# Kernel tuning notes

Hardware: AMD Instinct MI355X
Metric: run time of the kernel (lower is better)

## Reference

```python
import jax, jax.numpy as jnp
import numpy as np

NUM_PARAMS = 3  # stand-in for crit._num_params


def unfold(x, k):
    # torch F.unfold(kernel=(k,k), padding=k//2, stride=1) -> (N, C*k*k, H*W)
    # channel-major, then kh, then kw (matches torch ordering)
    N, C, H, W = x.shape
    p = k // 2
    xp = jnp.pad(x, ((0, 0), (0, 0), (p, p), (p, p)))
    cols = [xp[:, :, i:i + H, j:j + W] for i in range(k) for j in range(k)]
    return jnp.stack(cols, axis=2).reshape(N, C * k * k, H * W)


def conv1x1(x, w, b):
    return jnp.einsum('nchw,oc->nohw', x, w) + b[None, :, None, None]


def mlp_1x1(x, wa, ba, wb, bb, wc, bc):
    x = jax.nn.leaky_relu(conv1x1(x, wa, ba), 0.2)
    x = jax.nn.leaky_relu(conv1x1(x, wb, bb), 0.2)
    return conv1x1(x, wc, bc)


def crit(y, p):
    # Stand-in 3-parameter per-channel Gaussian criterion (weight-logit, mu, log-sigma).
    N, _, H, W = p.shape
    C = y.shape[1]
    p = p.reshape(N, NUM_PARAMS, C, H, W)
    w, mu, log_s = p[:, 0], p[:, 1], p[:, 2]
    log_s = jnp.clip(log_s, -7.0, 7.0)
    nll = 0.5 * ((y - mu) * jnp.exp(-log_s)) ** 2 + log_s + 0.9189385 - jax.nn.log_sigmoid(w)
    return nll  # (N, C, H, W)


def masked_conv5(x, w, b):
    # MaskedConv2d type 'A': zero center and everything after it in raster order
    k = w.shape[-1]
    m = jnp.ones((k, k), w.dtype)
    m = m.at[k // 2, k // 2:].set(0.0)
    m = m.at[k // 2 + 1:, :].set(0.0)
    out = jax.lax.conv_general_dilated(x, w * m, (1, 1), [(k // 2, k // 2)] * 2,
                                       dimension_numbers=('NCHW', 'OIHW', 'NCHW'))
    return out + b[None, :, None, None]


def conv_ref(ref_unfold, w, H, W):
    # Conv2dUnfold.forward: masked weight applied as matmul on unfolded patches; no bias, fold(1,1)
    O, C, kH, kW = w.shape
    m = jnp.ones((kH, kW), w.dtype)
    m = m.at[kH // 2, kW // 2 + 1:].set(0.0)  # center kept here
    m = m.at[kH // 2 + 1:, :].set(0.0)
    wm = (w * m).reshape(O, -1)
    out = jnp.einsum('oc,nci->noi', wm, ref_unfold)
    return out.reshape(ref_unfold.shape[0], O, H, W)


def search_transfer(y_hat, y_prob, k=3):
    N, C, H, W = y_hat.shape
    HW = H * W
    m = jnp.ones((C, k, k), y_hat.dtype)  # causal patch mask (center zeroed)
    m = m.at[:, k // 2, k // 2:].set(0.0)
    m = m.at[:, k // 2 + 1:, :].set(0.0)
    mask_unfold = m.reshape(1, C * k * k, 1)
    u = unfold(y_hat, k) * mask_unfold
    u = u / jnp.maximum(jnp.linalg.norm(u, axis=1, keepdims=True), 1e-12)
    R = jnp.einsum('nci,ncj->nij', u, u)        # (N, HW, HW) patch self-correlation
    R = jnp.triu(R, k=1)                        # eval mode: strictly earlier positions only
    R_star = R.max(axis=1)                      # (N, HW)
    R_arg = jnp.argmax(R, axis=1)               # (N, HW)
    y_unf = unfold(y_hat, k)                    # (N, C*k*k, HW)
    ref_unfold = jnp.take_along_axis(y_unf, R_arg[:, None, :], axis=2)
    U_unf = jnp.take_along_axis(y_prob.reshape(N, 1, HW), R_arg[:, None, :], axis=2)
    S = R_star.reshape(N, 1, H, W)
    U = U_unf.reshape(N, 1, H, W)
    # eval-mode fixups for the first (causal-less) position
    S = S.at[:, :, 0, 0].set(1e-8)
    U = U.at[:, :, 0, 0].set(1e-8)
    ref_unfold = ref_unfold.at[:, :, 0].set(0.0)
    R_arg = R_arg.at[:, 0].set(-1)
    S = jnp.clip(S, 1e-8, 1.0)
    U = jnp.clip(U, 1e-8, 1.0)
    return S, U, ref_unfold, R_arg


def setup_inputs():
    key = jax.random.key(0)
    ks = jax.random.split(key, 32)

    def rn(i, shape, s=1.0):
        return jax.random.normal(ks[i], shape, jnp.float32) * s

    C, CH, NP_, CHN = 128, 128, NUM_PARAMS, 128
    N, H, W = 4, 64, 64
    return dict(
        y_quant=rn(0, (N, C, H, W)),
        z_feature=rn(1, (N, CH, H, W)),
        w_mask5=rn(2, (2 * C, C, 5, 5), 0.02), b_mask5=rn(3, (2 * C,), 0.02),
        w1a=rn(4, (CHN, 2 * C), 0.05), b1a=rn(5, (CHN,), 0.02),
        w1b=rn(6, (CHN, CHN), 0.05), b1b=rn(7, (CHN,), 0.02),
        w1c=rn(8, (NP_ * C, CHN), 0.05), b1c=rn(9, (NP_ * C,), 0.02),
        w_ref=rn(10, (2 * C, C, 3, 3), 0.02),
        w2a=rn(11, (CHN, 4 * C), 0.05), b2a=rn(12, (CHN,), 0.02),
        w2b=rn(13, (CHN, CHN), 0.05), b2b=rn(14, (CHN,), 0.02),
        w2c=rn(15, (NP_ * C, CHN), 0.05), b2c=rn(16, (NP_ * C,), 0.02),
        w3a=rn(17, (CHN, 4 * C + CH), 0.05), b3a=rn(18, (CHN,), 0.02),
        w3b=rn(19, (CHN, CHN), 0.05), b3b=rn(20, (CHN,), 0.02),
        w3c=rn(21, (NP_ * C, CHN), 0.05), b3c=rn(22, (NP_ * C,), 0.02),
    )


def reference(y_quant, z_feature, w_mask5, b_mask5,
              w1a, b1a, w1b, b1b, w1c, b1c, w_ref,
              w2a, b2a, w2b, b2b, w2c, b2c,
              w3a, b3a, w3b, b3b, w3c, b3c):
    N, C, H, W = y_quant.shape
    sg = jax.lax.stop_gradient
    local = masked_conv5(y_quant, w_mask5, b_mask5)
    para1_det = mlp_1x1(sg(local), w1a, b1a, w1b, b1b, w1c, b1c)
    y_prob1 = jnp.exp(-crit(y_quant, para1_det)).mean(axis=1, keepdims=True)
    S, U, ref_unfold, R_arg = search_transfer(sg(y_quant), sg(y_prob1))
    ref_feature = conv_ref(ref_unfold, w_ref, H, W)
    para1 = mlp_1x1(local, w1a, b1a, w1b, b1b, w1c, b1c)
    para2 = mlp_1x1(jnp.concatenate([local, ref_feature], 1), w2a, b2a, w2b, b2b, w2c, b2c)
    para2 = para2.reshape(N, NUM_PARAMS, C, H, W)
    para2 = para2.at[:, 0].add(jnp.log(S + 1e-8) + jnp.log(U + 1e-8))  # broadcast over C
    para2 = para2.reshape(N, NUM_PARAMS * C, H, W)
    para3 = mlp_1x1(jnp.concatenate([local, ref_feature, z_feature], 1), w3a, b3a, w3b, b3b, w3c, b3c)
    return para1, para2, para3, S, U, R_arg
```

## Files before the change

kernel.cpp:

```cpp
#include <hip/hip_runtime.h>
#include <cstdint>
#include <cstddef>

typedef unsigned short ushort_t;
typedef __attribute__((ext_vector_type(8))) short bf16x8;
typedef __attribute__((ext_vector_type(4))) float f32x4;

#if defined(__has_builtin)
#if __has_builtin(__builtin_amdgcn_global_load_lds)
#define HAVE_GLL 1
#endif
#endif

constexpr int NB = 4;
constexpr size_t OUT_P1 = 0;
constexpr size_t OUT_P2 = 6291456;
constexpr size_t OUT_P3 = 12582912;
constexpr size_t OUT_S  = 18874368;
constexpr size_t OUT_U  = 18890752;
constexpr size_t OUT_RA = 18907136;

constexpr size_t WS_SS    = 0;
constexpr size_t WS_RNORM = 16384;
constexpr size_t WS_YPROB = 32768;
// ... 51 lines not shown
static __device__ inline void gll16(const ushort_t* g, ushort_t* l) {
#ifdef HAVE_GLL
    __builtin_amdgcn_global_load_lds((const __attribute__((address_space(1))) void*)g,
                                     (__attribute__((address_space(3))) void*)l, 16, 0, 0);
#else
    uint4 v = *(const uint4*)g;
    *(uint4*)((char*)l + (threadIdx.x & 63) * 16) = v;
#endif
}

#define MFMA3(AH, AL, BH, BL, ACC) \
    ACC = __builtin_amdgcn_mfma_f32_16x16x32_bf16(AH, BH, ACC, 0, 0, 0); \
    ACC = __builtin_amdgcn_mfma_f32_16x16x32_bf16(AH, BL, ACC, 0, 0, 0); \
    ACC = __builtin_amdgcn_mfma_f32_16x16x32_bf16(AL, BH, ACC, 0, 0, 0);

__global__ __launch_bounds__(256) void repack_split(
    const float* __restrict__ w5, const float* __restrict__ wr,
    const float* __restrict__ w1a, const float* __restrict__ w1b, const float* __restrict__ w1c,
    const float* __restrict__ w2a, const float* __restrict__ w2b, const float* __restrict__ w2c,
    const float* __restrict__ w3a, const float* __restrict__ w3b, const float* __restrict__ w3c,
    ushort_t* __restrict__ WH, ushort_t* __restrict__ WL)
{
    int idx = blockIdx.x * 256 + threadIdx.x;
    if (idx >= 933888) return;
    float v; int i = idx;
    if (i < 393216) {
        int o = i / 1536, k = i % 1536; int tp = k >> 7, c = k & 127;
        int f = (int)((ENC5 >> (5 * tp)) & 31); int dh = (f & 3) - 2, dw = ((f >> 2) & 7) - 2;
        v = w5[((size_t)(o * 128 + c)) * 25 + (dh + 2) * 5 + (dw + 2)];
    } else if ((i -= 393216) < 163840) {
        int o = i / 640, k = i % 640; int tp = k >> 7, c = k & 127;
        int f = (int)((ENC3 >> (5 * tp)) & 31); int dh = (f & 3) - 2, dw = ((f >> 2) & 7) - 2;
        v = wr[((size_t)(o * 128 + c)) * 9 + (dh + 1) * 3 + (dw + 1)];
    }
    else if ((i -= 163840) < 32768) v = w1a[i];
    else if ((i -= 32768) < 16384) v = w1b[i];
    else if ((i -= 16384) < 49152) v = w1c[i];
    else if ((i -= 49152) < 32768) { int o = i >> 8, k = i & 255; v = w2a[o * 512 + k]; }
    else if ((i -= 32768) < 32768) { int o = i >> 8, k = i & 255; v = w2a[o * 512 + 256 + k]; }
    else if ((i -= 32768) < 16384) v = w2b[i];
    else if ((i -= 16384) < 49152) v = w2c[i];
    else if ((i -= 49152) < 49152) { int o = i / 384, k = i % 384; v = (k < 256) ? w3a[o * 640 + k] : w3a[o * 640 + 512 + (k - 256)]; }
    else if ((i -= 49152) < 32768) { int o = i >> 8, k = i & 255; v = w3a[o * 640 + 256 + k]; }
    else if ((i -= 32768) < 16384) v = w3b[i];
    else { i -= 16384; v = w3c[i]; }
    ushort_t h = f2bf_rne(v);
    WH[idx] = h;
    WL[idx] = f2bf_rne(v - bf2f(h));
}

__global__ __launch_bounds__(256) void padclear(float* __restrict__ dst)
{
    size_t i = (size_t)blockIdx.x * 256 + threadIdx.x;
    ((uint4*)dst)[i] = uint4{0u, 0u, 0u, 0u};
}

__global__ __launch_bounds__(256) void transsplit(const float* __restrict__ src,
    ushort_t* __restrict__ dh, ushort_t* __restrict__ dl, int pad)
{
    __shared__ float tile[128][17];
    int wc = blockIdx.x, h = blockIdx.y, n = blockIdx.z;
    int t = threadIdx.x;
    {
        int tw = t & 15, tc = t >> 4;
        #pragma unroll
        for (int r = 0; r < 8; ++r) {
            int c = tc * 8 + r;
            tile[c][tw] = src[((size_t)(n * 128 + c) << 12) + (h << 6) + wc * 16 + tw];
        }
    }
    __syncthreads();
    {
        int cc = t & 127, ww = t >> 7;
        #pragma unroll
        for (int r = 0; r < 8; ++r) {
            int w = ww * 8 + r;
            float v = tile[cc][w];
            size_t drow = pad ? ((size_t)n * 4624 + (size_t)(h + 1) * 68 + wc * 16 + w + 1)
                              : ((size_t)n * 4096 + (h << 6) + wc * 16 + w);
            ushort_t hh = f2bf_rne(v);
            dh[drow * 128 + cc] = hh;
            dl[drow * 128 + cc] = f2bf_rne(v - bf2f(hh));
        }
    }
}

__global__ __launch_bounds__(256) void sumsq_kernel(const float* __restrict__ y, float* __restrict__ ws)
{
    int idx = blockIdx.x * 256 + threadIdx.x;
    int n = idx >> 12, p = idx & 4095;
    const float* yp = y + (size_t)n * 128 * 4096 + p;
    float s = 0.f;
    for (int c = 0; c < 128; ++c) { float v = yp[(size_t)c * 4096]; s += v * v; }
    ws[WS_SS + idx] = s;
}

__global__ __launch_bounds__(256) void rnorm_kernel(float* __restrict__ ws)
{
    int idx = blockIdx.x * 256 + threadIdx.x;
    int n = idx >> 12, p = idx & 4095;
    int h = p >> 6, w = p & 63;
    const float* ss = ws + WS_SS + ((size_t)n << 12);
    float nsq = 0.f;
    if (h > 0 && w > 0)  nsq += ss[p - 65];
    if (h > 0)           nsq += ss[p - 64];
    if (h > 0 && w < 63) nsq += ss[p - 63];
    if (w > 0)           nsq += ss[p - 1];
    ws[WS_RNORM + idx] = 1.0f / fmaxf(sqrtf(nsq), 1e-12f);
}

__global__ __launch_bounds__(256) void vbuild_kernel(const ushort_t* __restrict__ ytpH,
                                                     const ushort_t* __restrict__ ytpL,
                                                     float* __restrict__ ws)
{
    size_t idx = (size_t)blockIdx.x * 256 + threadIdx.x;
    int k = (int)(idx & 511);
    int j = (int)((idx >> 12) & 4095);
    int kj = (int)((idx >> 9) & 7);
    (void)kj;
    j = (int)((idx >> 9) & 4095);
    int n = (int)(idx >> 21);
    int tp = k >> 7, c = k & 127;
    int h = j >> 6, w = j & 63;
    int dh, dw;
    if      (tp == 0) { dh = -1; dw = -1; }
    else if (tp == 1) { dh = -1; dw = 0;  }
    else if (tp == 2) { dh = -1; dw = 1;  }
    else              { dh = 0;  dw = -1; }
    size_t row = (size_t)n * 4624 + (size_t)(h + 1 + dh) * 68 + (w + 1 + dw);
    float v = (bf2f(ytpH[row * 128 + c]) + bf2f(ytpL[row * 128 + c]))
              * ws[WS_RNORM + ((size_t)n << 12) + j];
    ushort_t hi = f2bf_rne(v);
    ushort_t lo = f2bf_rne(v - bf2f(hi));
    ((ushort_t*)(ws + WS_VH))[idx] = hi;
    ((ushort_t*)(ws + WS_VL))[idx] = lo;
}

__global__ __launch_bounds__(256) void gram_mfma(const ushort_t* __restrict__ VH,
                                                 const ushort_t* __restrict__ VL,
                                                 float* __restrict__ pmax, int* __restrict__ parg)
{
    __shared__ __align__(16) ushort_t AsH[128 * 32];
    __shared__ __align__(16) ushort_t AsL[128 * 32];
    __shared__ __align__(16) ushort_t BsH[128 * 32];
// ... 92 lines not shown
        if (lane < 16) {
            sredv[wq_i * 128 + wq_j * 64 + ni * 16 + lane] = bv;
            sredi[wq_i * 128 + wq_j * 64 + ni * 16 + lane] = bi;
        }
    }
    __syncthreads();
    if (t < 128) {
        float v0 = sredv[t]; int i0 = sredi[t];
        float v1 = sredv[128 + t]; int i1 = sredi[128 + t];
        if (v1 > v0) { v0 = v1; i0 = i1; }
        pmax[(((size_t)n * 32 + ib) << 12) + jb * 128 + t] = v0;
        parg[(((size_t)n * 32 + ib) << 12) + jb * 128 + t] = i0;
    }
}

__global__ __launch_bounds__(128) void mfma_conv(
    const ushort_t* __restrict__ WH, const ushort_t* __restrict__ WL,
    const float* __restrict__ bias,
    const ushort_t* __restrict__ YH, const ushort_t* __restrict__ YL,
    uint64_t tapenc, int Ktot,
    ushort_t* __restrict__ outH, ushort_t* __restrict__ outL)
{
    __shared__ __align__(16) ushort_t AsH[64 * 32], AsL[64 * 32];
    __shared__ __align__(16) ushort_t BsH[128 * 32], BsL[128 * 32];
    int t = threadIdx.x, w = t >> 6, lane = t & 63;
    int p0 = blockIdx.x << 7, o0 = blockIdx.y << 6, n = blockIdx.z;
    int colq = lane >> 2, ks = lane & 3;
    int fr = lane & 15, kg = lane >> 4;
    int h0 = p0 >> 6;
    const ushort_t* yh = YH + (size_t)n * 4624 * 128;
    const ushort_t* yl = YL + (size_t)n * 4624 * 128;

    const ushort_t* aSrcH0 = WH + (size_t)(o0 + (2 * w + 0) * 16 + colq) * Ktot + ks * 8;
    const ushort_t* aSrcH1 = WH + (size_t)(o0 + (2 * w + 1) * 16 + colq) * Ktot + ks * 8;
    const ushort_t* aSrcL0 = WL + (size_t)(o0 + (2 * w + 0) * 16 + colq) * Ktot + ks * 8;
    const ushort_t* aSrcL1 = WL + (size_t)(o0 + (2 * w + 1) * 16 + colq) * Ktot + ks * 8;

    f32x4 acc[4][4];
    #pragma unroll
    for (int mi = 0; mi < 4; ++mi)
        #pragma unroll
        for (int ni = 0; ni < 4; ++ni) acc[mi][ni] = (f32x4){0.f, 0.f, 0.f, 0.f};

    for (int k0 = 0; k0 < Ktot; k0 += 32) {
        int tp = k0 >> 7, coff = (k0 & 127) + ks * 8;
        int f = (int)((tapenc >> (5 * tp)) & 31);
        int dh = (f & 3) - 2, dw = ((f >> 2) & 7) - 2;
        gll16(aSrcH0 + k0, &AsH[(2 * w + 0) * 512]);
        gll16(aSrcH1 + k0, &AsH[(2 * w + 1) * 512]);
        gll16(aSrcL0 + k0, &AsL[(2 * w + 0) * 512]);
        gll16(aSrcL1 + k0, &AsL[(2 * w + 1) * 512]);
        #pragma unroll
        for (int cb = 0; cb < 4; ++cb) {
            int c = w * 64 + cb * 16 + colq;
            int prow = (h0 + (c >> 6) + 1 + dh) * 68 + (c & 63) + 1 + dw;
            gll16(yh + (size_t)prow * 128 + coff, &BsH[(w * 4 + cb) * 512]);
            gll16(yl + (size_t)prow * 128 + coff, &BsL[(w * 4 + cb) * 512]);
        }
#ifdef HAVE_GLL
        asm volatile("s_waitcnt vmcnt(0)" ::: "memory");
#endif
        __syncthreads();
        bf16x8 ah[4], al[4], bh[4], bl[4];
        #pragma unroll
        for (int mi = 0; mi < 4; ++mi) {
            int col = mi * 16 + fr;
            ah[mi] = *(const bf16x8*)&AsH[col * 32 + kg * 8];
            al[mi] = *(const bf16x8*)&AsL[col * 32 + kg * 8];
        }
        #pragma unroll
// ... 18 lines not shown
        if (bias) bv = *(const f32x4*)&bias[og];
        #pragma unroll
        for (int ni = 0; ni < 4; ++ni) {
            int p = p0 + w * 64 + ni * 16 + fr;
            f32x4 v = acc[mi][ni] + bv;
            ushort_t h0s = f2bf_rne(v[0]), h1s = f2bf_rne(v[1]), h2s = f2bf_rne(v[2]), h3s = f2bf_rne(v[3]);
            size_t db = (((size_t)n << 12) + p) * 256 + og;
            *(uint2*)&outH[db] = make_uint2(h0s | ((uint32_t)h1s << 16), h2s | ((uint32_t)h3s << 16));
            ushort_t l0s = f2bf_rne(v[0] - bf2f(h0s)), l1s = f2bf_rne(v[1] - bf2f(h1s));
            ushort_t l2s = f2bf_rne(v[2] - bf2f(h2s)), l3s = f2bf_rne(v[3] - bf2f(h3s));
            *(uint2*)&outL[db] = make_uint2(l0s | ((uint32_t)l1s << 16), l2s | ((uint32_t)l3s << 16));
        }
    }
}

__global__ __launch_bounds__(128) void mfma_dense(
    const ushort_t* __restrict__ WH, const ushort_t* __restrict__ WL,
    const ushort_t* __restrict__ B0H, const ushort_t* __restrict__ B0L, int str0,
    int Ktot, float* __restrict__ outF)
{
    __shared__ __align__(16) ushort_t AsH[64 * 32], AsL[64 * 32];
    __shared__ __align__(16) ushort_t BsH[128 * 32], BsL[128 * 32];
    int t = threadIdx.x, w = t >> 6, lane = t & 63;
    int p0 = blockIdx.x << 7, o0 = blockIdx.y << 6, n = blockIdx.z;
    int colq = lane >> 2, ks = lane & 3;
    int fr = lane & 15, kg = lane >> 4;

    const ushort_t* aSrcH0 = WH + (size_t)(o0 + (2 * w + 0) * 16 + colq) * Ktot + ks * 8;
    const ushort_t* aSrcH1 = WH + (size_t)(o0 + (2 * w + 1) * 16 + colq) * Ktot + ks * 8;
    const ushort_t* aSrcL0 = WL + (size_t)(o0 + (2 * w + 0) * 16 + colq) * Ktot + ks * 8;
    const ushort_t* aSrcL1 = WL + (size_t)(o0 + (2 * w + 1) * 16 + colq) * Ktot + ks * 8;
    size_t brow[4];
    #pragma unroll
    for (int cb = 0; cb < 4; ++cb)
        brow[cb] = ((size_t)n << 12) + p0 + w * 64 + cb * 16 + colq;

    f32x4 acc[4][4];
    #pragma unroll
    for (int mi = 0; mi < 4; ++mi)
        #pragma unroll
        for (int ni = 0; ni < 4; ++ni) acc[mi][ni] = (f32x4){0.f, 0.f, 0.f, 0.f};

    for (int k0 = 0; k0 < Ktot; k0 += 32) {
        gll16(aSrcH0 + k0, &AsH[(2 * w + 0) * 512]);
        gll16(aSrcH1 + k0, &AsH[(2 * w + 1) * 512]);
        gll16(aSrcL0 + k0, &AsL[(2 * w + 0) * 512]);
        gll16(aSrcL1 + k0, &AsL[(2 * w + 1) * 512]);
        int kk = k0 + ks * 8;
        #pragma unroll
        for (int cb = 0; cb < 4; ++cb) {
            gll16(B0H + brow[cb] * str0 + kk, &BsH[(w * 4 + cb) * 512]);
            gll16(B0L + brow[cb] * str0 + kk, &BsL[(w * 4 + cb) * 512]);
        }
#ifdef HAVE_GLL
        asm volatile("s_waitcnt vmcnt(0)" ::: "memory");
#endif
        __syncthreads();
        bf16x8 ah[4], al[4], bh[4], bl[4];
        #pragma unroll
        for (int mi = 0; mi < 4; ++mi) {
            int col = mi * 16 + fr;
            ah[mi] = *(const bf16x8*)&AsH[col * 32 + kg * 8];
            al[mi] = *(const bf16x8*)&AsL[col * 32 + kg * 8];
        }
        #pragma unroll
        for (int ni = 0; ni < 4; ++ni) {
            int col = w * 64 + ni * 16 + fr;
// ... 21 lines not shown
}

struct MlpCfg {
    const ushort_t *waH, *waL; const float* ba; int Ka;
    const ushort_t *wbH, *wbL; const float* bb;
    const ushort_t *wcH, *wcL; const float* bc;
    const ushort_t *x0H, *x0L; int k0len, str0;
    const ushort_t *x1H, *x1L; int str1;
    const float* gatherP; int addLsu;
    float* outBase;
};

__global__ __launch_bounds__(256) void mlp_fused(MlpCfg c0, MlpCfg c1,
    const int* __restrict__ argi, const float* __restrict__ lsu)
{
    __shared__ __align__(16) ushort_t hbH[16384];
    __shared__ __align__(16) ushort_t hbL[16384];
    const MlpCfg c = blockIdx.y ? c1 : c0;
    int t = threadIdx.x, lane = t & 63, w = t >> 6;
    int fr = lane & 15, kg = lane >> 4;
    int p0 = blockIdx.x << 7, n = blockIdx.z;

    {
        int o_t = w >> 1, p_h = w & 1;
        f32x4 acc[4][4];
        #pragma unroll
        for (int mi = 0; mi < 4; ++mi)
            #pragma unroll
            for (int ni = 0; ni < 4; ++ni) acc[mi][ni] = (f32x4){0.f, 0.f, 0.f, 0.f};
        for (int k0 = 0; k0 < c.Ka; k0 += 32) {
            const ushort_t *xh, *xl; int kk, str;
            if (k0 < c.k0len) { xh = c.x0H; xl = c.x0L; kk = k0; str = c.str0; }
            else              { xh = c.x1H; xl = c.x1L; kk = k0 - c.k0len; str = c.str1; }
            kk += kg * 8;
            bf16x8 ah[4], al[4], bh[4], bl[4];
            #pragma unroll
            for (int ni = 0; ni < 4; ++ni) {
                size_t row = ((size_t)n << 12) + p0 + p_h * 64 + ni * 16 + fr;
                bh[ni] = *(const bf16x8*)&xh[row * str + kk];
                bl[ni] = *(const bf16x8*)&xl[row * str + kk];
            }
            #pragma unroll
            for (int mi = 0; mi < 4; ++mi) {
                size_t orow = (size_t)(o_t * 64 + mi * 16 + fr) * c.Ka + k0 + kg * 8;
                ah[mi] = *(const bf16x8*)&c.waH[orow];
                al[mi] = *(const bf16x8*)&c.waL[orow];
            }
            #pragma unroll
            for (int mi = 0; mi < 4; ++mi)
                #pragma unroll
                for (int ni = 0; ni < 4; ++ni) {
                    MFMA3(ah[mi], al[mi], bh[ni], bl[ni], acc[mi][ni]);
                }
        }
        #pragma unroll
        for (int mi = 0; mi < 4; ++mi) {
            int og = o_t * 64 + mi * 16 + kg * 4;
            f32x4 bv = *(const f32x4*)&c.ba[og];
            #pragma unroll
            for (int ni = 0; ni < 4; ++ni) {
                int p_loc = p_h * 64 + ni * 16 + fr;
                int p = p0 + p_loc;
                f32x4 v = acc[mi][ni] + bv;
                if (c.gatherP) {
                    int aj = argi[(n << 12) + p];
                    if (aj >= 0) v += *(const f32x4*)&c.gatherP[(((size_t)n << 12) + aj) * 128 + og];
                }
                #pragma unroll
                for (int r = 0; r < 4; ++r) v[r] = v[r] > 0.f ? v[r] : 0.2f * v[r];
                int osw = og ^ ((p_loc & 7) << 3);
                ushort_t h0s = f2bf_rne(v[0]), h1s = f2bf_rne(v[1]), h2s = f2bf_rne(v[2]), h3s = f2bf_rne(v[3]);
                *(uint2*)&hbH[p_loc * 128 + osw] = make_uint2(h0s | ((uint32_t)h1s << 16), h2s | ((uint32_t)h3s << 16));
                ushort_t l0s = f2bf_rne(v[0] - bf2f(h0s)), l1s = f2bf_rne(v[1] - bf2f(h1s));
                ushort_t l2s = f2bf_rne(v[2] - bf2f(h2s)), l3s = f2bf_rne(v[3] - bf2f(h3s));
                *(uint2*)&hbL[p_loc * 128 + osw] = make_uint2(l0s | ((uint32_t)l1s << 16), l2s | ((uint32_t)l3s << 16));
            }
        }
    }
    __syncthreads();
    {
        int o_t = w >> 1, p_h = w & 1;
        f32x4 acc[4][4];
        #pragma unroll
        for (int mi = 0; mi < 4; ++mi)
            #pragma unroll
            for (int ni = 0; ni < 4; ++ni) acc[mi][ni] = (f32x4){0.f, 0.f, 0.f, 0.f};
        for (int k0 = 0; k0 < 128; k0 += 32) {
            bf16x8 ah[4], al[4], bh[4], bl[4];
            #pragma unroll
            for (int ni = 0; ni < 4; ++ni) {
                int p_loc = p_h * 64 + ni * 16 + fr;
                int koff = (k0 + kg * 8) ^ ((p_loc & 7) << 3);
                bh[ni] = *(const bf16x8*)&hbH[p_loc * 128 + koff];
                bl[ni] = *(const bf16x8*)&hbL[p_loc * 128 + koff];
            }
            #pragma unroll
            for (int mi = 0; mi < 4; ++mi) {
                size_t orow = (size_t)(o_t * 64 + mi * 16 + fr) * 128 + k0 + kg * 8;
                ah[mi] = *(const bf16x8*)&c.wbH[orow];
                al[mi] = *(const bf16x8*)&c.wbL[orow];
            }
            #pragma unroll
            for (int mi = 0; mi < 4; ++mi)
                #pragma unroll
                for (int ni = 0; ni < 4; ++ni) {
                    MFMA3(ah[mi], al[mi], bh[ni], bl[ni], acc[mi][ni]);
                }
        }
        __syncthreads();
        #pragma unroll
        for (int mi = 0; mi < 4; ++mi) {
            int og = o_t * 64 + mi * 16 + kg * 4;
            f32x4 bv = *(const f32x4*)&c.bb[og];
            #pragma unroll
            for (int ni = 0; ni < 4; ++ni) {
                int p_loc = p_h * 64 + ni * 16 + fr;
                f32x4 v = acc[mi][ni] + bv;
                #pragma unroll
                for (int r = 0; r < 4; ++r) v[r] = v[r] > 0.f ? v[r] : 0.2f * v[r];
                int osw = og ^ ((p_loc & 7) << 3);
                ushort_t h0s = f2bf_rne(v[0]), h1s = f2bf_rne(v[1]), h2s = f2bf_rne(v[2]), h3s = f2bf_rne(v[3]);
                *(uint2*)&hbH[p_loc * 128 + osw] = make_uint2(h0s | ((uint32_t)h1s << 16), h2s | ((uint32_t)h3s << 16));
                ushort_t l0s = f2bf_rne(v[0] - bf2f(h0s)), l1s = f2bf_rne(v[1] - bf2f(h1s));
                ushort_t l2s = f2bf_rne(v[2] - bf2f(h2s)), l3s = f2bf_rne(v[3] - bf2f(h3s));
                *(uint2*)&hbL[p_loc * 128 + osw] = make_uint2(l0s | ((uint32_t)l1s << 16), l2s | ((uint32_t)l3s << 16));
            }
        }
    }
    __syncthreads();
    for (int it = 0; it < 3; ++it) {
        int u = w + 4 * it;
        int o_t = u >> 1, p_h = u & 1;
        f32x4 acc[4][4];
        #pragma unroll
        for (int mi = 0; mi < 4; ++mi)
            #pragma unroll
            for (int ni = 0; ni < 4; ++ni) acc[mi][ni] = (f32x4){0.f, 0.f, 0.f, 0.f};
        for (int k0 = 0; k0 < 128; k0 += 32) {
            bf16x8 ah[4], al[4], bh[4], bl[4];
            #pragma unroll
            for (int ni = 0; ni < 4; ++ni) {
                int p_loc = p_h * 64 + ni * 16 + fr;
                int koff = (k0 + kg * 8) ^ ((p_loc & 7) << 3);
                bh[ni] = *(const bf16x8*)&hbH[p_loc * 128 + koff];
                bl[ni] = *(const bf16x8*)&hbL[p_loc * 128 + koff];
            }
            #pragma unroll
            for (int mi = 0; mi < 4; ++mi) {
                size_t orow = (size_t)(o_t * 64 + mi * 16 + fr) * 128 + k0 + kg * 8;
                ah[mi] = *(const bf16x8*)&c.wcH[orow];
                al[mi] = *(const bf16x8*)&c.wcL[orow];
            }
            #pragma unroll
            for (int mi = 0; mi < 4; ++mi)
                #pragma unroll
                for (int ni = 0; ni < 4; ++ni) {
                    MFMA3(ah[mi], al[mi], bh[ni], bl[ni], acc[mi][ni]);
                }
        }
        #pragma unroll
        for (int mi = 0; mi < 4; ++mi) {
            int og = o_t * 64 + mi * 16 + kg * 4;
            f32x4 bv = *(const f32x4*)&c.bc[og];
            #pragma unroll
            for (int ni = 0; ni < 4; ++ni) {
                int p = p0 + p_h * 64 + ni * 16 + fr;
                f32x4 v = acc[mi][ni] + bv;
                if (c.addLsu && og < 128) {
                    float lv = lsu[(n << 12) + p];
                    v[0] += lv; v[1] += lv; v[2] += lv; v[3] += lv;
                }
                float* dst = c.outBase + (((size_t)(n * 384 + og)) << 12) + p;
                dst[0] = v[0]; dst[4096] = v[1]; dst[8192] = v[2]; dst[12288] = v[3];
            }
        }
    }
}

__global__ __launch_bounds__(256) void yprob_kernel(
    const float* __restrict__ out, const float* __restrict__ y, float* __restrict__ ws)
{
    int idx = blockIdx.x * 256 + threadIdx.x;
    int n = idx >> 12, p = idx & 4095;
    const float* pw = out + OUT_P1 + (size_t)n * 384 * 4096 + p;
    const float* pm = pw + (size_t)128 * 4096;
    const float* psv = pm + (size_t)128 * 4096;
    const float* yy = y + (size_t)n * 128 * 4096 + p;
    float accs = 0.f;
    for (int c = 0; c < 128; ++c) {
        float w  = pw[(size_t)c * 4096];
        float mu = pm[(size_t)c * 4096];
        float ls = psv[(size_t)c * 4096];
        ls = fminf(fmaxf(ls, -7.f), 7.f);
        float tt = (yy[(size_t)c * 4096] - mu) * expf(-ls);
        float lsig = (w >= 0.f) ? -log1pf(expf(-w)) : (w - log1pf(expf(w)));
        float nll = 0.5f * tt * tt + ls + 0.9189385f - lsig;
        accs += expf(-nll);
    }
    ws[WS_YPROB + idx] = accs * (1.0f / 128.0f);
}

__global__ __launch_bounds__(256) void finalize_kernel(float* __restrict__ ws, float* __restrict__ out)
{
    int idx = blockIdx.x * 256 + threadIdx.x;
    int n = idx >> 12, j = idx & 4095;
    float s, u; int a;
    if (j == 0) { s = 1e-8f; u = 1e-8f; a = -1; }
    else {
        float bv = -INFINITY; int bi = 0x7fffffff;
        const int* pai = (const int*)ws;
        int jbt = j >> 7;
        for (int ib = 0; ib <= jbt; ++ib) {
            float v = ws[WS_PMAX + (((size_t)n * 32 + ib) << 12) + j];
            int ii = pai[WS_PARG + (((size_t)n * 32 + ib) << 12) + j];
// ... 44 lines not shown
    const int* argi = (const int*)(ws) + WS_ARGI;

    ushort_t* wph = (ushort_t*)(ws + WS_WPK);
    ushort_t* wpl = wph + 933888;
    ushort_t* locH = (ushort_t*)(ws + WS_LOCH);
    ushort_t* locL = (ushort_t*)(ws + WS_LOCL);
    ushort_t* ftH  = (ushort_t*)(ws + WS_FTH);
    ushort_t* ftL  = (ushort_t*)(ws + WS_FTL);
    float* p2t = ws + WS_P2T;
    float* p3t = ws + WS_P3T;
    ushort_t* ztpH = (ushort_t*)(ws + WS_ZTPH);
    ushort_t* ztpL = (ushort_t*)(ws + WS_ZTPL);
    ushort_t* ytpH = (ushort_t*)(out + OS_YTPH);
    ushort_t* ytpL = (ushort_t*)(out + OS_YTPL);

    repack_split<<<3648, 256, 0, stream>>>(w5, wrf, w1a, w1b, w1c, w2a, w2b, w2c, w3a, w3b, w3c, wph, wpl);
    padclear<<<2312, 256, 0, stream>>>(out + OS_YTPH);
    transsplit<<<dim3(4, 64, NB), 256, 0, stream>>>(y, ytpH, ytpL, 1);
    transsplit<<<dim3(4, 64, NB), 256, 0, stream>>>(z, ztpH, ztpL, 0);
    sumsq_kernel<<<64, 256, 0, stream>>>(y, ws);
    rnorm_kernel<<<64, 256, 0, stream>>>(ws);
    vbuild_kernel<<<32768, 256, 0, stream>>>(ytpH, ytpL, ws);
    gram_mfma<<<dim3(528, NB), 256, 0, stream>>>((const ushort_t*)(ws + WS_VH), (const ushort_t*)(ws + WS_VL),
                                                 ws + WS_PMAX, (int*)(ws + WS_PARG));

    mfma_conv<<<dim3(32, 4, NB), 128, 0, stream>>>(wph + WP_W5, wpl + WP_W5, b5, ytpH, ytpL, ENC5, 1536, locH, locL);
    mfma_conv<<<dim3(32, 4, NB), 128, 0, stream>>>(wph + WP_WR, wpl + WP_WR, nullptr, ytpH, ytpL, ENC3, 640, ftH, ftL);
    mfma_dense<<<dim3(32, 2, NB), 128, 0, stream>>>(wph + WP_W2AR, wpl + WP_W2AR, ftH, ftL, 256, 256, p2t);
    mfma_dense<<<dim3(32, 2, NB), 128, 0, stream>>>(wph + WP_W3AR, wpl + WP_W3AR, ftH, ftL, 256, 256, p3t);

    MlpCfg m1;
    m1.waH = wph + WP_W1A; m1.waL = wpl + WP_W1A; m1.ba = b1a; m1.Ka = 256;
    m1.wbH = wph + WP_W1B; m1.wbL = wpl + WP_W1B; m1.bb = b1b;
    m1.wcH = wph + WP_W1C; m1.wcL = wpl + WP_W1C; m1.bc = b1c;
    m1.x0H = locH; m1.x0L = locL; m1.k0len = 256; m1.str0 = 256;
    m1.x1H = locH; m1.x1L = locL; m1.str1 = 256;
    m1.gatherP = nullptr; m1.addLsu = 0; m1.outBase = out + OUT_P1;
    mlp_fused<<<dim3(32, 1, NB), 256, 0, stream>>>(m1, m1, argi, ws + WS_LSU);

    yprob_kernel<<<64, 256, 0, stream>>>(out, y, ws);
    finalize_kernel<<<64, 256, 0, stream>>>(ws, out);

    MlpCfg m2;
    m2.waH = wph + WP_W2AL; m2.waL = wpl + WP_W2AL; m2.ba = b2a; m2.Ka = 256;
    m2.wbH = wph + WP_W2B; m2.wbL = wpl + WP_W2B; m2.bb = b2b;
    m2.wcH = wph + WP_W2C; m2.wcL = wpl + WP_W2C; m2.bc = b2c;
    m2.x0H = locH; m2.x0L = locL; m2.k0len = 256; m2.str0 = 256;
    m2.x1H = locH; m2.x1L = locL; m2.str1 = 256;
    m2.gatherP = p2t; m2.addLsu = 1; m2.outBase = out + OUT_P2;
    MlpCfg m3;
    m3.waH = wph + WP_W3ALZ; m3.waL = wpl + WP_W3ALZ; m3.ba = b3a; m3.Ka = 384;
    m3.wbH = wph + WP_W3B; m3.wbL = wpl + WP_W3B; m3.bb = b3b;
    m3.wcH = wph + WP_W3C; m3.wcL = wpl + WP_W3C; m3.bc = b3c;
    m3.x0H = locH; m3.x0L = locL; m3.k0len = 256; m3.str0 = 256;
    m3.x1H = ztpH; m3.x1L = ztpL; m3.str1 = 128;
    m3.gatherP = p3t; m3.addLsu = 0; m3.outBase = out + OUT_P3;
    mlp_fused<<<dim3(32, 2, NB), 256, 0, stream>>>(m2, m3, argi, ws + WS_LSU);

    (void)in_sizes; (void)n_in; (void)out_size; (void)ws_size;
}
```

Before: 623.4 us.

## Merge prep and conv launches, widen reductions, halve MLP tile for more blocks

Fuses the weight repack, pad clearing and both transposes into one prep kernel, clearing only the border rows of a now 2-wide padded y buffer. Merges the two conv GEMMs and the two dense GEMMs into single launches. Splits the sumsq and yprob channel reductions across four thread groups with a shared-memory reduction and a grid four times larger. Halves the MLP pixel tile to double the grid and cut LDS use. The goal is fewer launches and better GPU occupancy on these small kernels, at the cost of extra index logic and per-block weight reloads in the MLP.

Result: faster. 517.8 us (-16.9%).

```diff
diff --git a/kernel.cpp b/kernel.cpp
--- a/kernel.cpp
+++ b/kernel.cpp
@@ -89,53 +89,65 @@
     ACC = __builtin_amdgcn_mfma_f32_16x16x32_bf16(AH, BL, ACC, 0, 0, 0); \
     ACC = __builtin_amdgcn_mfma_f32_16x16x32_bf16(AL, BH, ACC, 0, 0, 0);
 
-__global__ __launch_bounds__(256) void repack_split(
+__global__ __launch_bounds__(256) void prep_fused(
     const float* __restrict__ w5, const float* __restrict__ wr,
     const float* __restrict__ w1a, const float* __restrict__ w1b, const float* __restrict__ w1c,
     const float* __restrict__ w2a, const float* __restrict__ w2b, const float* __restrict__ w2c,
     const float* __restrict__ w3a, const float* __restrict__ w3b, const float* __restrict__ w3c,
-    ushort_t* __restrict__ WH, ushort_t* __restrict__ WL)
-{
-    int idx = blockIdx.x * 256 + threadIdx.x;
-    if (idx >= 933888) return;
-    float v; int i = idx;
-    if (i < 393216) {
-        int o = i / 1536, k = i % 1536; int tp = k >> 7, c = k & 127;
-        int f = (int)((ENC5 >> (5 * tp)) & 31); int dh = (f & 3) - 2, dw = ((f >> 2) & 7) - 2;
-        v = w5[((size_t)(o * 128 + c)) * 25 + (dh + 2) * 5 + (dw + 2)];
-    } else if ((i -= 393216) < 163840) {
-        int o = i / 640, k = i % 640; int tp = k >> 7, c = k & 127;
-        int f = (int)((ENC3 >> (5 * tp)) & 31); int dh = (f & 3) - 2, dw = ((f >> 2) & 7) - 2;
-        v = wr[((size_t)(o * 128 + c)) * 9 + (dh + 1) * 3 + (dw + 1)];
-    }
-    else if ((i -= 163840) < 32768) v = w1a[i];
-    else if ((i -= 32768) < 16384) v = w1b[i];
-    else if ((i -= 16384) < 49152) v = w1c[i];
-    else if ((i -= 49152) < 32768) { int o = i >> 8, k = i & 255; v = w2a[o * 512 + k]; }
-    else if ((i -= 32768) < 32768) { int o = i >> 8, k = i & 255; v = w2a[o * 512 + 256 + k]; }
-    else if ((i -= 32768) < 16384) v = w2b[i];
-    else if ((i -= 16384) < 49152) v = w2c[i];
-    else if ((i -= 49152) < 49152) { int o = i / 384, k = i % 384; v = (k < 256) ? w3a[o * 640 + k] : w3a[o * 640 + 512 + (k - 256)]; }
-    else if ((i -= 49152) < 32768) { int o = i >> 8, k = i & 255; v = w3a[o * 640 + 256 + k]; }
-    else if ((i -= 32768) < 16384) v = w3b[i];
-    else { i -= 16384; v = w3c[i]; }
-    ushort_t h = f2bf_rne(v);
-    WH[idx] = h;
-    WL[idx] = f2bf_rne(v - bf2f(h));
-}
-
-__global__ __launch_bounds__(256) void padclear(float* __restrict__ dst)
-{
-    size_t i = (size_t)blockIdx.x * 256 + threadIdx.x;
-    ((uint4*)dst)[i] = uint4{0u, 0u, 0u, 0u};
-}
-
-__global__ __launch_bounds__(256) void transsplit(const float* __restrict__ src,
-    ushort_t* __restrict__ dh, ushort_t* __restrict__ dl, int pad)
+    const float* __restrict__ y, const float* __restrict__ z,
+    ushort_t* __restrict__ WH, ushort_t* __restrict__ WL,
+    ushort_t* __restrict__ ytpH, ushort_t* __restrict__ ytpL,
+    ushort_t* __restrict__ ztpH, ushort_t* __restrict__ ztpL)
 {
     __shared__ float tile[128][17];
-    int wc = blockIdx.x, h = blockIdx.y, n = blockIdx.z;
-    int t = threadIdx.x;
+    int b = blockIdx.x, t = threadIdx.x;
+    if (b < 3648) {
+        int idx = b * 256 + t;
+        if (idx >= 933888) return;
+        float v; int i = idx;
+        if (i < 393216) {
+            int o = i / 1536, k = i % 1536; int tp = k >> 7, c = k & 127;
+            int f = (int)((ENC5 >> (5 * tp)) & 31); int dh = (f & 3) - 2, dw = ((f >> 2) & 7) - 2;
+            v = w5[((size_t)(o * 128 + c)) * 25 + (dh + 2) * 5 + (dw + 2)];
+        } else if ((i -= 393216) < 163840) {
+            int o = i / 640, k = i % 640; int tp = k >> 7, c = k & 127;
+            int f = (int)((ENC3 >> (5 * tp)) & 31); int dh = (f & 3) - 2, dw = ((f >> 2) & 7) - 2;
+            v = wr[((size_t)(o * 128 + c)) * 9 + (dh + 1) * 3 + (dw + 1)];
+        }
+        else if ((i -= 163840) < 32768) v = w1a[i];
+        else if ((i -= 32768) < 16384) v = w1b[i];
+        else if ((i -= 16384) < 49152) v = w1c[i];
+        else if ((i -= 49152) < 32768) { int o = i >> 8, k = i & 255; v = w2a[o * 512 + k]; }
+        else if ((i -= 32768) < 32768) { int o = i >> 8, k = i & 255; v = w2a[o * 512 + 256 + k]; }
+        else if ((i -= 32768) < 16384) v = w2b[i];
+        else if ((i -= 16384) < 49152) v = w2c[i];
+        else if ((i -= 49152) < 49152) { int o = i / 384, k = i % 384; v = (k < 256) ? w3a[o * 640 + k] : w3a[o * 640 + 512 + (k - 256)]; }
+        else if ((i -= 49152) < 32768) { int o = i >> 8, k = i & 255; v = w3a[o * 640 + 256 + k]; }
+        else if ((i -= 32768) < 16384) v = w3b[i];
+        else { i -= 16384; v = w3c[i]; }
+        ushort_t h = f2bf_rne(v);
+        WH[idx] = h;
+        WL[idx] = f2bf_rne(v - bf2f(h));
+        return;
+    }
+    if (b < 3912) {
+        int slot = (b - 3648) * 8 + (t >> 5);
+        int n = slot / 528, rp = slot % 528;
+        int r, wcol;
+        if (rp < 272) { int x = rp / 68; r = x + ((x >> 1) << 6); wcol = rp % 68; }
+        else { int q = rp - 272; r = 2 + (q >> 2); int x = q & 3; wcol = x + ((x >> 1) << 6); }
+        size_t row = (size_t)n * 4624 + (size_t)r * 68 + wcol;
+        int lane = t & 31;
+        ushort_t* dst = ((lane >> 4) ? ytpL : ytpH) + row * 128;
+        ((uint4*)dst)[lane & 15] = uint4{0u, 0u, 0u, 0u};
+        return;
+    }
+    int b2, pad;
+    const float* src;
+    ushort_t *dh_, *dl_;
+    if (b < 4936) { b2 = b - 3912; pad = 1; src = y; dh_ = ytpH; dl_ = ytpL; }
+    else          { b2 = b - 4936; pad = 0; src = z; dh_ = ztpH; dl_ = ztpL; }
+    int wc = b2 & 3, h = (b2 >> 2) & 63, n = b2 >> 8;
     {
         int tw = t & 15, tc = t >> 4;
         #pragma unroll
@@ -151,23 +163,30 @@
         for (int r = 0; r < 8; ++r) {
             int w = ww * 8 + r;
             float v = tile[cc][w];
-            size_t drow = pad ? ((size_t)n * 4624 + (size_t)(h + 1) * 68 + wc * 16 + w + 1)
+            size_t drow = pad ? ((size_t)n * 4624 + (size_t)(h + 2) * 68 + wc * 16 + w + 2)
                               : ((size_t)n * 4096 + (h << 6) + wc * 16 + w);
             ushort_t hh = f2bf_rne(v);
-            dh[drow * 128 + cc] = hh;
-            dl[drow * 128 + cc] = f2bf_rne(v - bf2f(hh));
+            dh_[drow * 128 + cc] = hh;
+            dl_[drow * 128 + cc] = f2bf_rne(v - bf2f(hh));
         }
     }
 }
 
 __global__ __launch_bounds__(256) void sumsq_kernel(const float* __restrict__ y, float* __restrict__ ws)
 {
-    int idx = blockIdx.x * 256 + threadIdx.x;
-    int n = idx >> 12, p = idx & 4095;
-    const float* yp = y + (size_t)n * 128 * 4096 + p;
+    __shared__ float red[4][64];
+    int n = blockIdx.y, t = threadIdx.x;
+    int pl = t & 63, cg = t >> 6;
+    int p = (blockIdx.x << 6) + pl;
+    const float* yp = y + ((size_t)(n * 128 + cg * 32) << 12) + p;
     float s = 0.f;
-    for (int c = 0; c < 128; ++c) { float v = yp[(size_t)c * 4096]; s += v * v; }
-    ws[WS_SS + idx] = s;
+    #pragma unroll 8
+    for (int c = 0; c < 32; ++c) { float v = yp[(size_t)c << 12]; s = fmaf(v, v, s); }
+    red[cg][pl] = s;
+    __syncthreads();
+    if (t < 64)
+        ws[WS_SS + ((size_t)n << 12) + (blockIdx.x << 6) + t] =
+            red[0][t] + red[1][t] + red[2][t] + red[3][t];
 }
 
 __global__ __launch_bounds__(256) void rnorm_kernel(float* __restrict__ ws)
@@ -190,10 +209,7 @@
 {
     size_t idx = (size_t)blockIdx.x * 256 + threadIdx.x;
     int k = (int)(idx & 511);
-    int j = (int)((idx >> 12) & 4095);
-    int kj = (int)((idx >> 9) & 7);
-    (void)kj;
-    j = (int)((idx >> 9) & 4095);
+    int j = (int)((idx >> 9) & 4095);
     int n = (int)(idx >> 21);
     int tp = k >> 7, c = k & 127;
     int h = j >> 6, w = j & 63;
@@ -202,7 +218,7 @@
     else if (tp == 1) { dh = -1; dw = 0;  }
     else if (tp == 2) { dh = -1; dw = 1;  }
     else              { dh = 0;  dw = -1; }
-    size_t row = (size_t)n * 4624 + (size_t)(h + 1 + dh) * 68 + (w + 1 + dw);
+    size_t row = (size_t)n * 4624 + (size_t)(h + 2 + dh) * 68 + (w + 2 + dw);
     float v = (bf2f(ytpH[row * 128 + c]) + bf2f(ytpL[row * 128 + c]))
               * ws[WS_RNORM + ((size_t)n << 12) + j];
     ushort_t hi = f2bf_rne(v);
@@ -325,17 +341,28 @@
     }
 }
 
-__global__ __launch_bounds__(128) void mfma_conv(
-    const ushort_t* __restrict__ WH, const ushort_t* __restrict__ WL,
-    const float* __restrict__ bias,
+__global__ __launch_bounds__(128) void conv_merged(
+    const ushort_t* __restrict__ W5H, const ushort_t* __restrict__ W5L, const float* __restrict__ b5,
+    const ushort_t* __restrict__ WrH, const ushort_t* __restrict__ WrL,
     const ushort_t* __restrict__ YH, const ushort_t* __restrict__ YL,
-    uint64_t tapenc, int Ktot,
-    ushort_t* __restrict__ outH, ushort_t* __restrict__ outL)
+    ushort_t* __restrict__ locH, ushort_t* __restrict__ locL,
+    ushort_t* __restrict__ ftH, ushort_t* __restrict__ ftL)
 {
     __shared__ __align__(16) ushort_t AsH[64 * 32], AsL[64 * 32];
     __shared__ __align__(16) ushort_t BsH[128 * 32], BsL[128 * 32];
+    int by = blockIdx.y;
+    bool is5 = by < 4;
+    const ushort_t* WH = is5 ? W5H : WrH;
+    const ushort_t* WL = is5 ? W5L : WrL;
+    const float* bias = is5 ? b5 : nullptr;
+    uint64_t tapenc = is5 ? ENC5 : ENC3;
+    int Ktot = is5 ? 1536 : 640;
+    ushort_t* outH = is5 ? locH : ftH;
+    ushort_t* outL = is5 ? locL : ftL;
+    int o0 = (is5 ? by : by - 4) << 6;
+
     int t = threadIdx.x, w = t >> 6, lane = t & 63;
-    int p0 = blockIdx.x << 7, o0 = blockIdx.y << 6, n = blockIdx.z;
+    int p0 = blockIdx.x << 7, n = blockIdx.z;
     int colq = lane >> 2, ks = lane & 3;
     int fr = lane & 15, kg = lane >> 4;
     int h0 = p0 >> 6;
@@ -364,7 +391,7 @@
         #pragma unroll
         for (int cb = 0; cb < 4; ++cb) {
             int c = w * 64 + cb * 16 + colq;
-            int prow = (h0 + (c >> 6) + 1 + dh) * 68 + (c & 63) + 1 + dw;
+            int prow = (h0 + (c >> 6) + 2 + dh) * 68 + (c & 63) + 2 + dw;
             gll16(yh + (size_t)prow * 128 + coff, &BsH[(w * 4 + cb) * 512]);
             gll16(yl + (size_t)prow * 128 + coff, &BsL[(w * 4 + cb) * 512]);
         }
@@ -413,15 +440,23 @@
     }
 }
 
-__global__ __launch_bounds__(128) void mfma_dense(
-    const ushort_t* __restrict__ WH, const ushort_t* __restrict__ WL,
-    const ushort_t* __restrict__ B0H, const ushort_t* __restrict__ B0L, int str0,
-    int Ktot, float* __restrict__ outF)
+__global__ __launch_bounds__(128) void dense_merged(
+    const ushort_t* __restrict__ W2H, const ushort_t* __restrict__ W2L,
+    const ushort_t* __restrict__ W3H, const ushort_t* __restrict__ W3L,
+    const ushort_t* __restrict__ B0H, const ushort_t* __restrict__ B0L,
+    float* __restrict__ p2t, float* __restrict__ p3t)
 {
     __shared__ __align__(16) ushort_t AsH[64 * 32], AsL[64 * 32];
     __shared__ __align__(16) ushort_t BsH[128 * 32], BsL[128 * 32];
+    int by = blockIdx.y;
+    const ushort_t* WH = (by < 2) ? W2H : W3H;
+    const ushort_t* WL = (by < 2) ? W2L : W3L;
+    float* outF = (by < 2) ? p2t : p3t;
+    int o0 = (by & 1) << 6;
+    constexpr int Ktot = 256;
+
     int t = threadIdx.x, w = t >> 6, lane = t & 63;
-    int p0 = blockIdx.x << 7, o0 = blockIdx.y << 6, n = blockIdx.z;
+    int p0 = blockIdx.x << 7, n = blockIdx.z;
     int colq = lane >> 2, ks = lane & 3;
     int fr = lane & 15, kg = lane >> 4;
 
@@ -448,8 +483,8 @@
         int kk = k0 + ks * 8;
         #pragma unroll
         for (int cb = 0; cb < 4; ++cb) {
-            gll16(B0H + brow[cb] * str0 + kk, &BsH[(w * 4 + cb) * 512]);
-            gll16(B0L + brow[cb] * str0 + kk, &BsL[(w * 4 + cb) * 512]);
+            gll16(B0H + brow[cb] * 256 + kk, &BsH[(w * 4 + cb) * 512]);
+            gll16(B0L + brow[cb] * 256 + kk, &BsL[(w * 4 + cb) * 512]);
         }
 #ifdef HAVE_GLL
         asm volatile("s_waitcnt vmcnt(0)" ::: "memory");
@@ -501,29 +536,29 @@
 __global__ __launch_bounds__(256) void mlp_fused(MlpCfg c0, MlpCfg c1,
     const int* __restrict__ argi, const float* __restrict__ lsu)
 {
-    __shared__ __align__(16) ushort_t hbH[16384];
-    __shared__ __align__(16) ushort_t hbL[16384];
+    __shared__ __align__(16) ushort_t hbH[8192];
+    __shared__ __align__(16) ushort_t hbL[8192];
     const MlpCfg c = blockIdx.y ? c1 : c0;
     int t = threadIdx.x, lane = t & 63, w = t >> 6;
     int fr = lane & 15, kg = lane >> 4;
-    int p0 = blockIdx.x << 7, n = blockIdx.z;
+    int p0 = blockIdx.x << 6, n = blockIdx.z;
+    int o_t = w >> 1, p_h = w & 1;
 
     {
-        int o_t = w >> 1, p_h = w & 1;
-        f32x4 acc[4][4];
+        f32x4 acc[4][2];
         #pragma unroll
         for (int mi = 0; mi < 4; ++mi)
             #pragma unroll
-            for (int ni = 0; ni < 4; ++ni) acc[mi][ni] = (f32x4){0.f, 0.f, 0.f, 0.f};
+            for (int ni = 0; ni < 2; ++ni) acc[mi][ni] = (f32x4){0.f, 0.f, 0.f, 0.f};
         for (int k0 = 0; k0 < c.Ka; k0 += 32) {
             const ushort_t *xh, *xl; int kk, str;
             if (k0 < c.k0len) { xh = c.x0H; xl = c.x0L; kk = k0; str = c.str0; }
             else              { xh = c.x1H; xl = c.x1L; kk = k0 - c.k0len; str = c.str1; }
             kk += kg * 8;
-            bf16x8 ah[4], al[4], bh[4], bl[4];
-            #pragma unroll
-            for (int ni = 0; ni < 4; ++ni) {
-                size_t row = ((size_t)n << 12) + p0 + p_h * 64 + ni * 16 + fr;
+            bf16x8 ah[4], al[4], bh[2], bl[2];
+            #pragma unroll
+            for (int ni = 0; ni < 2; ++ni) {
+                size_t row = ((size_t)n << 12) + p0 + p_h * 32 + ni * 16 + fr;
                 bh[ni] = *(const bf16x8*)&xh[row * str + kk];
                 bl[ni] = *(const bf16x8*)&xl[row * str + kk];
             }
@@ -536,7 +571,7 @@
             #pragma unroll
             for (int mi = 0; mi < 4; ++mi)
                 #pragma unroll
-                for (int ni = 0; ni < 4; ++ni) {
+                for (int ni = 0; ni < 2; ++ni) {
                     MFMA3(ah[mi], al[mi], bh[ni], bl[ni], acc[mi][ni]);
                 }
         }
@@ -545,8 +580,8 @@
             int og = o_t * 64 + mi * 16 + kg * 4;
             f32x4 bv = *(const f32x4*)&c.ba[og];
             #pragma unroll
-            for (int ni = 0; ni < 4; ++ni) {
-                int p_loc = p_h * 64 + ni * 16 + fr;
+            for (int ni = 0; ni < 2; ++ni) {
+                int p_loc = p_h * 32 + ni * 16 + fr;
                 int p = p0 + p_loc;
                 f32x4 v = acc[mi][ni] + bv;
                 if (c.gatherP) {
@@ -566,17 +601,16 @@
     }
     __syncthreads();
     {
-        int o_t = w >> 1, p_h = w & 1;
-        f32x4 acc[4][4];
+        f32x4 acc[4][2];
         #pragma unroll
         for (int mi = 0; mi < 4; ++mi)
             #pragma unroll
-            for (int ni = 0; ni < 4; ++ni) acc[mi][ni] = (f32x4){0.f, 0.f, 0.f, 0.f};
+            for (int ni = 0; ni < 2; ++ni) acc[mi][ni] = (f32x4){0.f, 0.f, 0.f, 0.f};
         for (int k0 = 0; k0 < 128; k0 += 32) {
-            bf16x8 ah[4], al[4], bh[4], bl[4];
-            #pragma unroll
-            for (int ni = 0; ni < 4; ++ni) {
-                int p_loc = p_h * 64 + ni * 16 + fr;
+            bf16x8 ah[4], al[4], bh[2], bl[2];
+            #pragma unroll
+            for (int ni = 0; ni < 2; ++ni) {
+                int p_loc = p_h * 32 + ni * 16 + fr;
                 int koff = (k0 + kg * 8) ^ ((p_loc & 7) << 3);
                 bh[ni] = *(const bf16x8*)&hbH[p_loc * 128 + koff];
                 bl[ni] = *(const bf16x8*)&hbL[p_loc * 128 + koff];
@@ -590,7 +624,7 @@
             #pragma unroll
             for (int mi = 0; mi < 4; ++mi)
                 #pragma unroll
-                for (int ni = 0; ni < 4; ++ni) {
+                for (int ni = 0; ni < 2; ++ni) {
                     MFMA3(ah[mi], al[mi], bh[ni], bl[ni], acc[mi][ni]);
                 }
         }
@@ -600,8 +634,8 @@
             int og = o_t * 64 + mi * 16 + kg * 4;
             f32x4 bv = *(const f32x4*)&c.bb[og];
             #pragma unroll
-            for (int ni = 0; ni < 4; ++ni) {
-                int p_loc = p_h * 64 + ni * 16 + fr;
+            for (int ni = 0; ni < 2; ++ni) {
+                int p_loc = p_h * 32 + ni * 16 + fr;
                 f32x4 v = acc[mi][ni] + bv;
                 #pragma unroll
                 for (int r = 0; r < 4; ++r) v[r] = v[r] > 0.f ? v[r] : 0.2f * v[r];
@@ -617,41 +651,41 @@
     __syncthreads();
     for (int it = 0; it < 3; ++it) {
         int u = w + 4 * it;
-        int o_t = u >> 1, p_h = u & 1;
-        f32x4 acc[4][4];
+        int o3 = u >> 1, p3 = u & 1;
+        f32x4 acc[4][2];
         #pragma unroll
         for (int mi = 0; mi < 4; ++mi)
             #pragma unroll
-            for (int ni = 0; ni < 4; ++ni) acc[mi][ni] = (f32x4){0.f, 0.f, 0.f, 0.f};
+            for (int ni = 0; ni < 2; ++ni) acc[mi][ni] = (f32x4){0.f, 0.f, 0.f, 0.f};
         for (int k0 = 0; k0 < 128; k0 += 32) {
-            bf16x8 ah[4], al[4], bh[4], bl[4];
-            #pragma unroll
-            for (int ni = 0; ni < 4; ++ni) {
-                int p_loc = p_h * 64 + ni * 16 + fr;
+            bf16x8 ah[4], al[4], bh[2], bl[2];
+            #pragma unroll
+            for (int ni = 0; ni < 2; ++ni) {
+                int p_loc = p3 * 32 + ni * 16 + fr;
                 int koff = (k0 + kg * 8) ^ ((p_loc & 7) << 3);
                 bh[ni] = *(const bf16x8*)&hbH[p_loc * 128 + koff];
                 bl[ni] = *(const bf16x8*)&hbL[p_loc * 128 + koff];
             }
             #pragma unroll
             for (int mi = 0; mi < 4; ++mi) {
-                size_t orow = (size_t)(o_t * 64 + mi * 16 + fr) * 128 + k0 + kg * 8;
+                size_t orow = (size_t)(o3 * 64 + mi * 16 + fr) * 128 + k0 + kg * 8;
                 ah[mi] = *(const bf16x8*)&c.wcH[orow];
                 al[mi] = *(const bf16x8*)&c.wcL[orow];
             }
             #pragma unroll
             for (int mi = 0; mi < 4; ++mi)
                 #pragma unroll
-                for (int ni = 0; ni < 4; ++ni) {
+                for (int ni = 0; ni < 2; ++ni) {
                     MFMA3(ah[mi], al[mi], bh[ni], bl[ni], acc[mi][ni]);
                 }
         }
         #pragma unroll
         for (int mi = 0; mi < 4; ++mi) {
-            int og = o_t * 64 + mi * 16 + kg * 4;
+            int og = o3 * 64 + mi * 16 + kg * 4;
             f32x4 bv = *(const f32x4*)&c.bc[og];
             #pragma unroll
-            for (int ni = 0; ni < 4; ++ni) {
-                int p = p0 + p_h * 64 + ni * 16 + fr;
+            for (int ni = 0; ni < 2; ++ni) {
+                int p = p0 + p3 * 32 + ni * 16 + fr;
                 f32x4 v = acc[mi][ni] + bv;
                 if (c.addLsu && og < 128) {
                     float lv = lsu[(n << 12) + p];
@@ -667,24 +701,31 @@
 __global__ __launch_bounds__(256) void yprob_kernel(
     const float* __restrict__ out, const float* __restrict__ y, float* __restrict__ ws)
 {
-    int idx = blockIdx.x * 256 + threadIdx.x;
-    int n = idx >> 12, p = idx & 4095;
-    const float* pw = out + OUT_P1 + (size_t)n * 384 * 4096 + p;
-    const float* pm = pw + (size_t)128 * 4096;
-    const float* psv = pm + (size_t)128 * 4096;
-    const float* yy = y + (size_t)n * 128 * 4096 + p;
-    float accs = 0.f;
-    for (int c = 0; c < 128; ++c) {
-        float w  = pw[(size_t)c * 4096];
-        float mu = pm[(size_t)c * 4096];
-        float ls = psv[(size_t)c * 4096];
+    __shared__ float red[4][64];
+    int n = blockIdx.y, t = threadIdx.x;
+    int pl = t & 63, cg = t >> 6;
+    int p = (blockIdx.x << 6) + pl;
+    const float* bw = out + OUT_P1 + ((size_t)(n * 384 + cg * 32) << 12) + p;
+    const float* bm = bw + ((size_t)128 << 12);
+    const float* bs = bm + ((size_t)128 << 12);
+    const float* by_ = y + ((size_t)(n * 128 + cg * 32) << 12) + p;
+    float acc = 0.f;
+    for (int cc = 0; cc < 32; ++cc) {
+        float w  = bw[(size_t)cc << 12];
+        float mu = bm[(size_t)cc << 12];
+        float ls = bs[(size_t)cc << 12];
+        float yv = by_[(size_t)cc << 12];
         ls = fminf(fmaxf(ls, -7.f), 7.f);
-        float tt = (yy[(size_t)c * 4096] - mu) * expf(-ls);
+        float tt = (yv - mu) * expf(-ls);
         float lsig = (w >= 0.f) ? -log1pf(expf(-w)) : (w - log1pf(expf(w)));
         float nll = 0.5f * tt * tt + ls + 0.9189385f - lsig;
-        accs += expf(-nll);
-    }
-    ws[WS_YPROB + idx] = accs * (1.0f / 128.0f);
+        acc += expf(-nll);
+    }
+    red[cg][pl] = acc;
+    __syncthreads();
+    if (t < 64)
+        ws[WS_YPROB + ((size_t)n << 12) + (blockIdx.x << 6) + t] =
+            (red[0][t] + red[1][t] + red[2][t] + red[3][t]) * (1.0f / 128.0f);
 }
 
 __global__ __launch_bounds__(256) void finalize_kernel(float* __restrict__ ws, float* __restrict__ out)
@@ -759,20 +800,20 @@
     ushort_t* ytpH = (ushort_t*)(out + OS_YTPH);
     ushort_t* ytpL = (ushort_t*)(out + OS_YTPL);
 
-    repack_split<<<3648, 256, 0, stream>>>(w5, wrf, w1a, w1b, w1c, w2a, w2b, w2c, w3a, w3b, w3c, wph, wpl);
-    padclear<<<2312, 256, 0, stream>>>(out + OS_YTPH);
-    transsplit<<<dim3(4, 64, NB), 256, 0, stream>>>(y, ytpH, ytpL, 1);
-    transsplit<<<dim3(4, 64, NB), 256, 0, stream>>>(z, ztpH, ztpL, 0);
-    sumsq_kernel<<<64, 256, 0, stream>>>(y, ws);
+    prep_fused<<<5960, 256, 0, stream>>>(w5, wrf, w1a, w1b, w1c, w2a, w2b, w2c, w3a, w3b, w3c,
+                                         y, z, wph, wpl, ytpH, ytpL, ztpH, ztpL);
+    sumsq_kernel<<<dim3(64, NB), 256, 0, stream>>>(y, ws);
     rnorm_kernel<<<64, 256, 0, stream>>>(ws);
     vbuild_kernel<<<32768, 256, 0, stream>>>(ytpH, ytpL, ws);
     gram_mfma<<<dim3(528, NB), 256, 0, stream>>>((const ushort_t*)(ws + WS_VH), (const ushort_t*)(ws + WS_VL),
                                                  ws + WS_PMAX, (int*)(ws + WS_PARG));
 
-    mfma_conv<<<dim3(32, 4, NB), 128, 0, stream>>>(wph + WP_W5, wpl + WP_W5, b5, ytpH, ytpL, ENC5, 1536, locH, locL);
-    mfma_conv<<<dim3(32, 4, NB), 128, 0, stream>>>(wph + WP_WR, wpl + WP_WR, nullptr, ytpH, ytpL, ENC3, 640, ftH, ftL);
-    mfma_dense<<<dim3(32, 2, NB), 128, 0, stream>>>(wph + WP_W2AR, wpl + WP_W2AR, ftH, ftL, 256, 256, p2t);
-    mfma_dense<<<dim3(32, 2, NB), 128, 0, stream>>>(wph + WP_W3AR, wpl + WP_W3AR, ftH, ftL, 256, 256, p3t);
+    conv_merged<<<dim3(32, 8, NB), 128, 0, stream>>>(wph + WP_W5, wpl + WP_W5, b5,
+                                                     wph + WP_WR, wpl + WP_WR,
+                                                     ytpH, ytpL, locH, locL, ftH, ftL);
+    dense_merged<<<dim3(32, 4, NB), 128, 0, stream>>>(wph + WP_W2AR, wpl + WP_W2AR,
+                                                      wph + WP_W3AR, wpl + WP_W3AR,
+                                                      ftH, ftL, p2t, p3t);
 
     MlpCfg m1;
     m1.waH = wph + WP_W1A; m1.waL = wpl + WP_W1A; m1.ba = b1a; m1.Ka = 256;
@@ -781,9 +822,9 @@
     m1.x0H = locH; m1.x0L = locL; m1.k0len = 256; m1.str0 = 256;
     m1.x1H = locH; m1.x1L = locL; m1.str1 = 256;
     m1.gatherP = nullptr; m1.addLsu = 0; m1.outBase = out + OUT_P1;
-    mlp_fused<<<dim3(32, 1, NB), 256, 0, stream>>>(m1, m1, argi, ws + WS_LSU);
-
-    yprob_kernel<<<64, 256, 0, stream>>>(out, y, ws);
+    mlp_fused<<<dim3(64, 1, NB), 256, 0, stream>>>(m1, m1, argi, ws + WS_LSU);
+
+    yprob_kernel<<<dim3(64, NB), 256, 0, stream>>>(out, y, ws);
     finalize_kernel<<<64, 256, 0, stream>>>(ws, out);
 
     MlpCfg m2;
@@ -800,7 +841,7 @@
     m3.x0H = locH; m3.x0L = locL; m3.k0len = 256; m3.str0 = 256;
     m3.x1H = ztpH; m3.x1L = ztpL; m3.str1 = 128;
     m3.gatherP = p3t; m3.addLsu = 0; m3.outBase = out + OUT_P3;
-    mlp_fused<<<dim3(32, 2, NB), 256, 0, stream>>>(m2, m3, argi, ws + WS_LSU);
+    mlp_fused<<<dim3(64, 2, NB), 256, 0, stream>>>(m2, m3, argi, ws + WS_LSU);
 
     (void)in_sizes; (void)n_in; (void)out_size; (void)ws_size;
 }
```
